# Optimization experiments

Measured on AMD Instinct MI355X. Metric: run time of the kernel, lower is better.

Reference implementation:

```python
import jax, jax.numpy as jnp
import numpy as np


def setup_inputs() -> dict:
    key = jax.random.key(0)
    ks = jax.random.split(key, 9)
    B, C, H, W = 16, 512, 56, 56
    I = C // 2
    return {
        "x": jax.random.normal(ks[0], (B, C, H, W), dtype=jnp.float32),
        "g_w": jax.random.normal(ks[1], (I, C), dtype=jnp.float32) * 0.02,
        "g_b": jax.random.normal(ks[2], (I,), dtype=jnp.float32) * 0.02,
        "theta_w": jax.random.normal(ks[3], (I, C), dtype=jnp.float32) * 0.02,
        "theta_b": jax.random.normal(ks[4], (I,), dtype=jnp.float32) * 0.02,
        "phi_w": jax.random.normal(ks[5], (I, C), dtype=jnp.float32) * 0.02,
        "phi_b": jax.random.normal(ks[6], (I,), dtype=jnp.float32) * 0.02,
        "W_w": jax.random.normal(ks[7], (C, I), dtype=jnp.float32) * 0.02,
        "W_b": jax.random.normal(ks[8], (C,), dtype=jnp.float32) * 0.02,
    }


def reference(x, g_w, g_b, theta_w, theta_b, phi_w, phi_b, W_w, W_b):
    B, C, H, W = x.shape
    N = H * W
    xf = x.reshape(B, C, N)  # flatten spatial -> [B, C, N]
    # 1x1 convs == per-pixel channel matmuls
    g = jnp.einsum('ic,bcn->bin', g_w, xf) + g_b[:, None]        # [B, I, N]
    th = jnp.einsum('ic,bcn->bin', theta_w, xf) + theta_b[:, None]
    ph = jnp.einsum('ic,bcn->bin', phi_w, xf) + phi_b[:, None]
    # Original: y = (theta^T @ phi / N) @ g^T. No softmax -> reassociate:
    # y = theta^T @ ((phi @ g^T) / N), avoiding the [B, N, N] score matrix.
    M = jnp.einsum('bjn,bin->bji', ph, g) / N                    # [B, I, I]
    y = jnp.einsum('bjn,bji->bin', th, M)                        # [B, I, N]
    out = jnp.einsum('ci,bin->bcn', W_w, y) + W_b[:, None]       # [B, C, N]
    return x + out.reshape(B, C, H, W)
```

## Files before the change

### kernel.cpp

```cpp
#include <hip/hip_runtime.h>
#include <stdint.h>


typedef unsigned short ushort_t;
typedef __attribute__((ext_vector_type(8))) short short8;
typedef __attribute__((ext_vector_type(4))) float f32x4;
typedef __attribute__((ext_vector_type(4))) unsigned short us4;
typedef __attribute__((ext_vector_type(8))) unsigned short us8;

#define NSP  3136
#define XNR  3200
#define PLD  3200

#define AS1(p) ((const __attribute__((address_space(1))) void*)(p))
#define AS3(p) ((__attribute__((address_space(3))) void*)(p))

__device__ inline ushort_t f2b(float f) {
  union { float f; uint32_t u; } c; c.f = f;
  uint32_t u = c.u;
  uint32_t r = (u + 0x7fffu + ((u >> 16) & 1u)) >> 16;
  return (ushort_t)r;
}

__global__ __launch_bounds__(512, 2) void g1_8phase(
    const ushort_t* __restrict__ W3,
    const ushort_t* __restrict__ xbase,
    ushort_t* __restrict__ P,
    ushort_t* __restrict__ thT,
    const float* __restrict__ bias)
{
  const int nwg = gridDim.x * gridDim.y * gridDim.z;
  int flat = blockIdx.x + gridDim.x * (blockIdx.y + gridDim.y * blockIdx.z);
  const int q = nwg >> 3;
  int swz = (flat & 7) * q + (flat >> 3);
  const int bx = swz % gridDim.x; int tmp = swz / gridDim.x;
  const int by = tmp % gridDim.y;
  const int b  = tmp / gridDim.y;

  const int m0 = bx * 256;
  const int n0 = by * 256;
  const ushort_t* Ag = W3;
  const ushort_t* Bg = xbase + (size_t)b * XNR * 512;

  const int tid = threadIdx.x;
  const int lane = tid & 63;
  const int wid = tid >> 6;
  const int wm = wid >> 2;
  const int wn = wid & 3;
  const int fr = lane & 15;
  const int fk = lane >> 4;
  const int hB = wn >> 1;
  const int rB0 = (wn & 1) * 64;
  const int s0 = ((fk) ^ (fr & 7)) * 8;
  const int s1 = ((4 | fk) ^ (fr & 7)) * 8;
  const int rth = tid >> 3;
  const int swc = ((tid & 7) ^ ((tid >> 3) & 7)) * 8;

  __shared__ __align__(16) ushort_t SM[65536];
  ushort_t (*As)[2][8192] = (ushort_t(*)[2][8192])(SM);
  ushort_t (*Bs)[2][8192] = (ushort_t(*)[2][8192])(SM + 32768);

  f32x4 acc[8][4];
#pragma unroll
  for (int i = 0; i < 8; ++i)
#pragma unroll
    for (int j = 0; j < 4; ++j) acc[i][j] = f32x4{0.f, 0.f, 0.f, 0.f};

#define STG_A(h, kt, BUF) do { \
    const ushort_t* s_ = Ag + (size_t)(m0 + (h) * 128 + rth) * 512 + (kt) * 64 + swc; \
    __builtin_amdgcn_global_load_lds(AS1(s_), AS3(&As[BUF][h][tid * 8]), 16, 0, 0); \
    __builtin_amdgcn_global_load_lds(AS1(s_ + 64 * 512), AS3(&As[BUF][h][4096 + tid * 8]), 16, 0, 0); \
  } while (0)
#define STG_B(h, kt, BUF) do { \
    const ushort_t* s_ = Bg + (size_t)(n0 + (h) * 128 + rth) * 512 + (kt) * 64 + swc; \
    __builtin_amdgcn_global_load_lds(AS1(s_), AS3(&Bs[BUF][h][tid * 8]), 16, 0, 0); \
    __builtin_amdgcn_global_load_lds(AS1(s_ + 64 * 512), AS3(&Bs[BUF][h][4096 + tid * 8]), 16, 0, 0); \
  } while (0)

#define BARR __builtin_amdgcn_s_barrier()
#define LGKM0 do { asm volatile("s_waitcnt lgkmcnt(0)" ::: "memory"); \
                   __builtin_amdgcn_sched_barrier(0); } while (0)
#define MF16(AF, BF, OFS) do { \
    __builtin_amdgcn_s_setprio(1); \
    _Pragma("unroll") for (int mf_ = 0; mf_ < 4; ++mf_) \
    _Pragma("unroll") for (int nf_ = 0; nf_ < 4; ++nf_) \
      acc[(OFS) + mf_][nf_] = __builtin_amdgcn_mfma_f32_16x16x32_bf16( \
          AF[mf_], BF[nf_], acc[(OFS) + mf_][nf_], 0, 0, 0); \
    __builtin_amdgcn_s_setprio(0); \
  } while (0)

#define TILE(T, CUR, DO_B1, DO_T2, VMN) do { \
    short8 a0[4], a1[4], a2[4], a3[4], b0[4], b1[4]; \
    _Pragma("unroll") for (int i = 0; i < 4; ++i) \
      a0[i] = *(const short8*)&As[CUR][wm][(i * 16 + fr) * 64 + s0]; \
    _Pragma("unroll") for (int i = 0; i < 4; ++i) \
      b0[i] = *(const short8*)&Bs[CUR][hB][(rB0 + i * 16 + fr) * 64 + s0]; \
    if (DO_B1) STG_B(1, (T) + 1, (CUR) ^ 1); \
    BARR; LGKM0; MF16(a0, b0, 0); BARR; \
    _Pragma("unroll") for (int i = 0; i < 4; ++i) \
      a1[i] = *(const short8*)&As[CUR][wm][((i + 4) * 16 + fr) * 64 + s0]; \
    _Pragma("unroll") for (int i = 0; i < 4; ++i) \
      b1[i] = *(const short8*)&Bs[CUR][hB][(rB0 + i * 16 + fr) * 64 + s1]; \
    BARR; LGKM0; MF16(a1, b0, 4); BARR; \
    _Pragma("unroll") for (int i = 0; i < 4; ++i) \
      a2[i] = *(const short8*)&As[CUR][wm][(i * 16 + fr) * 64 + s1]; \
    _Pragma("unroll") for (int i = 0; i < 4; ++i) \
      a3[i] = *(const short8*)&As[CUR][wm][((i + 4) * 16 + fr) * 64 + s1]; \
    if (DO_T2) STG_B(0, (T) + 2, (CUR)); \
    BARR; LGKM0; MF16(a2, b1, 0); BARR; \
    if (DO_T2) { STG_A(0, (T) + 2, (CUR)); STG_A(1, (T) + 2, (CUR)); } \
    if ((VMN) == 6) asm volatile("s_waitcnt vmcnt(6)" ::: "memory"); \
    else if ((VMN) == 0) asm volatile("s_waitcnt vmcnt(0)" ::: "memory"); \
    BARR; MF16(a3, b1, 4); BARR; \
  } while (0)

  asm volatile("s_waitcnt vmcnt(0)" ::: "memory");
  STG_A(0, 0, 0); STG_A(1, 0, 0); STG_B(0, 0, 0); STG_B(1, 0, 0);
  STG_B(0, 1, 1); STG_A(0, 1, 1); STG_A(1, 1, 1);
  asm volatile("s_waitcnt vmcnt(6)" ::: "memory");
  BARR;

  for (int t = 0; t < 6; t += 2) { TILE(t, 0, 1, 1, 6); TILE(t + 1, 1, 1, 1, 6); }
  TILE(6, 0, 1, 0, 0);
  TILE(7, 1, 0, 0, -1);

#undef TILE
#undef STG_A
#undef STG_B

  if (m0 == 512) {
#pragma unroll
    for (int p = 0; p < 2; ++p) {
      if ((wn >> 1) == p) {
        const int lcb = (wn & 1) * 64;
#pragma unroll
        for (int m = 0; m < 8; ++m) {
          int jr = wm * 128 + m * 16 + fk * 4;
#pragma unroll
          for (int n = 0; n < 4; ++n) {
            int lc = lcb + n * 16 + fr;
            us4 o;
#pragma unroll
            for (int r = 0; r < 4; ++r) o[r] = f2b(acc[m][n][r] + bias[512 + jr + r]);
            *reinterpret_cast<us4*>(&SM[lc * 264 + jr]) = o;
          }
        }
      }
      BARR;
#pragma unroll
      for (int it = 0; it < 8; ++it) {
        int idx = it * 512 + tid;
        int lc = idx >> 5, ch = idx & 31;
        int col = n0 + p * 128 + lc;
        if (col < NSP)
          *reinterpret_cast<us8*>(&thT[((size_t)b * NSP + col) * 256 + ch * 8]) =
              *reinterpret_cast<const us8*>(&SM[lc * 264 + ch * 8]);
      }
      BARR;
    }
  } else {
    us8 z = {0, 0, 0, 0, 0, 0, 0, 0};
#pragma unroll
    for (int p = 0; p < 2; ++p) {
      if (wm == p) {
#pragma unroll
        for (int m = 0; m < 8; ++m) {
#pragma unroll
          for (int n = 0; n < 4; ++n) {
            int col = wn * 64 + n * 16 + fr;
#pragma unroll
            for (int r = 0; r < 4; ++r) {
              int lrow = m * 16 + fk * 4 + r;
              SM[lrow * 264 + col] = f2b(acc[m][n][r] + bias[m0 + p * 128 + lrow]);
            }
          }
        }
      }
      BARR;
#pragma unroll
      for (int it = 0; it < 8; ++it) {
        int idx = it * 512 + tid;
        int row = idx >> 5, ch = idx & 31;
        int gcol = n0 + ch * 8;
        if (gcol < PLD) {
          us8 v = (gcol < NSP) ? *reinterpret_cast<const us8*>(&SM[row * 264 + ch * 8]) : z;
          *reinterpret_cast<us8*>(
              &P[(size_t)b * 512 * PLD + (size_t)(m0 + p * 128 + row) * PLD + gcol]) = v;
        }
      }
      BARR;
    }
  }
}

template<int MODE>
__global__ __launch_bounds__(256, 2) void gemm64(
    const ushort_t* __restrict__ Abase,
    const ushort_t* __restrict__ Bbase,
    void* __restrict__ Cbase,
    const float* __restrict__ bias,
    const float* __restrict__ xres)
{
  constexpr int TB = 256;
  constexpr int MR = 4;
  constexpr int WN = 2;
  constexpr int CH = TB / 8;

  const int nwg = gridDim.x * gridDim.y * gridDim.z;
  int flat = blockIdx.x + gridDim.x * (blockIdx.y + gridDim.y * blockIdx.z);
  const int q = nwg >> 3;
  int swz = (flat & 7) * q + (flat >> 3);
  const int bx = swz % gridDim.x; int tmp = swz / gridDim.x;
  const int by = tmp % gridDim.y;
  const int bz = tmp / gridDim.y;

  int b, kc = 0, kbeg, kend, lda, ldb;
  const ushort_t *A, *B;
  if constexpr (MODE == 2) {
    b = bz & 15; kc = bz >> 4;
    A = Abase + (size_t)b * 512 * PLD + (size_t)256 * PLD;
    B = Abase + (size_t)b * 512 * PLD;
    lda = PLD; ldb = PLD; kbeg = kc * 640; kend = kbeg + 640;
  } else if constexpr (MODE == 6) {
    b = bz; A = Abase; lda = 256;
    B = Bbase + (size_t)b * 65536; ldb = 256;
    kbeg = 0; kend = 256;
  } else {
    b = bz; A = Abase + (size_t)b * 131072; lda = 256;
    B = Bbase + (size_t)b * NSP * 256; ldb = 256;
    kbeg = 0; kend = 256;
  }

  const int m0 = bx * 128;
  const int n0 = by * 128;
  const int tid = threadIdx.x;
  const int lane = tid & 63;
  const int wid = tid >> 6;
  const int wm = wid / WN, wn = wid % WN;
  const int fr = lane & 15;
  const int fk = lane >> 4;

  __shared__ __align__(16) ushort_t As[2][128 * 64];
  __shared__ __align__(16) ushort_t Bs[2][128 * 64];

  f32x4 acc[MR][4];
#pragma unroll
  for (int i = 0; i < MR; ++i)
#pragma unroll
    for (int j = 0; j < 4; ++j) acc[i][j] = f32x4{0.f, 0.f, 0.f, 0.f};

  const int srow = tid >> 3;
  const int lsl = (tid & 7) ^ (srow & 7);
  const ushort_t* pa = A + (size_t)(m0 + srow) * lda + kbeg + lsl * 8;
  const ushort_t* pb = B + (size_t)(n0 + srow) * ldb + kbeg + lsl * 8;

#define STAGE(bufi) do {                                                              \
    __builtin_amdgcn_global_load_lds(AS1(pa),                    AS3(&As[bufi][tid * 8]), 16, 0, 0); \
    __builtin_amdgcn_global_load_lds(AS1(pa + (size_t)CH * lda), AS3(&As[bufi][TB * 8 + tid * 8]), 16, 0, 0); \
    __builtin_amdgcn_global_load_lds(AS1(pa + (size_t)2 * CH * lda), AS3(&As[bufi][2 * TB * 8 + tid * 8]), 16, 0, 0); \
    __builtin_amdgcn_global_load_lds(AS1(pa + (size_t)3 * CH * lda), AS3(&As[bufi][3 * TB * 8 + tid * 8]), 16, 0, 0); \
    __builtin_amdgcn_global_load_lds(AS1(pb),                    AS3(&Bs[bufi][tid * 8]), 16, 0, 0); \
    __builtin_amdgcn_global_load_lds(AS1(pb + (size_t)CH * ldb), AS3(&Bs[bufi][TB * 8 + tid * 8]), 16, 0, 0); \
    __builtin_amdgcn_global_load_lds(AS1(pb + (size_t)2 * CH * ldb), AS3(&Bs[bufi][2 * TB * 8 + tid * 8]), 16, 0, 0); \
    __builtin_amdgcn_global_load_lds(AS1(pb + (size_t)3 * CH * ldb), AS3(&Bs[bufi][3 * TB * 8 + tid * 8]), 16, 0, 0); \
    pa += 64; pb += 64;                                                               \
  } while (0)

  const int sw = fr & 7;
  const int s0 = ((0 | fk) ^ sw) * 8;
  const int s1 = ((4 | fk) ^ sw) * 8;
  const int arow = (wm * MR * 16 + fr) * 64;
  const int brow = (wn * 64 + fr) * 64;

  asm volatile("s_waitcnt vmcnt(0)" ::: "memory");
  STAGE(0);

  const int nkt = (kend - kbeg) >> 6;
  for (int t = 0; t < nkt; ++t) {
    const int cur = t & 1;
    if (t + 1 < nkt) {
      STAGE(cur ^ 1);
      asm volatile("s_waitcnt vmcnt(8)" ::: "memory");
    } else {
      asm volatile("s_waitcnt vmcnt(0)" ::: "memory");
    }
    __builtin_amdgcn_s_barrier();
    __builtin_amdgcn_sched_barrier(0);

    short8 bf[4][2];
#pragma unroll
    for (int n = 0; n < 4; ++n) {
      bf[n][0] = *reinterpret_cast<const short8*>(&Bs[cur][brow + n * 1024 + s0]);
      bf[n][1] = *reinterpret_cast<const short8*>(&Bs[cur][brow + n * 1024 + s1]);
    }
    short8 af[4][2];
#pragma unroll
    for (int m = 0; m < 4; ++m) {
      af[m][0] = *reinterpret_cast<const short8*>(&As[cur][arow + m * 1024 + s0]);
      af[m][1] = *reinterpret_cast<const short8*>(&As[cur][arow + m * 1024 + s1]);
    }
    __builtin_amdgcn_s_setprio(1);
#pragma unroll
    for (int m = 0; m < 4; ++m)
#pragma unroll
      for (int n = 0; n < 4; ++n) {
        acc[m][n] = __builtin_amdgcn_mfma_f32_16x16x32_bf16(af[m][0], bf[n][0], acc[m][n], 0, 0, 0);
        acc[m][n] = __builtin_amdgcn_mfma_f32_16x16x32_bf16(af[m][1], bf[n][1], acc[m][n], 0, 0, 0);
      }
    __builtin_amdgcn_s_setprio(0);
    __builtin_amdgcn_s_barrier();
  }
#undef STAGE

  if constexpr (MODE == 2) {
    float* Mf = (float*)Cbase;
#pragma unroll
    for (int m = 0; m < MR; ++m)
#pragma unroll
      for (int n = 0; n < 4; ++n) {
        int gcol = n0 + wn * 64 + n * 16 + fr;
#pragma unroll
        for (int r = 0; r < 4; ++r) {
          int grow = m0 + wm * 64 + m * 16 + fk * 4 + r;
          Mf[((size_t)kc * 16 + b) * 65536 + grow * 256 + gcol] = acc[m][n][r];
        }
      }
  } else if constexpr (MODE == 6) {
    ushort_t* U = (ushort_t*)Cbase;
#pragma unroll
    for (int m = 0; m < MR; ++m)
#pragma unroll
      for (int n = 0; n < 4; ++n) {
        int gcol = n0 + wn * 64 + n * 16 + fr;
#pragma unroll
        for (int r = 0; r < 4; ++r) {
          int grow = m0 + wm * 64 + m * 16 + fk * 4 + r;
          U[(size_t)b * 131072 + grow * 256 + gcol] = f2b(acc[m][n][r]);
        }
      }
  } else {
    float* out = (float*)Cbase;
#pragma unroll
    for (int m = 0; m < MR; ++m)
#pragma unroll
      for (int n = 0; n < 4; ++n) {
        int gcol = n0 + wn * 64 + n * 16 + fr;
        if (gcol < NSP) {
#pragma unroll
          for (int r = 0; r < 4; ++r) {
            int grow = m0 + wm * 64 + m * 16 + fk * 4 + r;
            size_t o = ((size_t)b * 512 + grow) * NSP + gcol;
            out[o] = acc[m][n][r] + bias[grow] + xres[o];
          }
        }
      }
  }
}

__global__ __launch_bounds__(256) void transp_x(const float* __restrict__ x,
                                                ushort_t* __restrict__ xb)
{
  const int nt = blockIdx.x, ct = blockIdx.y, b = blockIdx.z;
  const int t = threadIdx.x;
  const int n0 = nt * 64, c0 = ct * 64;
  __shared__ float Ls[64 * 65];

  const float* xs = x + (size_t)b * 512 * NSP;
#pragma unroll
  for (int p = 0; p < 4; ++p) {
    int cl = p * 16 + (t >> 4);
    int nl = (t & 15) * 4;
    f32x4 v = *reinterpret_cast<const f32x4*>(&xs[(size_t)(c0 + cl) * NSP + n0 + nl]);
    Ls[cl * 65 + nl + 0] = v[0];
    Ls[cl * 65 + nl + 1] = v[1];
    Ls[cl * 65 + nl + 2] = v[2];
    Ls[cl * 65 + nl + 3] = v[3];
  }
  __syncthreads();
#pragma unroll
  for (int it = 0; it < 2; ++it) {
    int idx = it * 256 + t; int nl = idx >> 3, cc = idx & 7;
    us8 o;
#pragma unroll
    for (int j = 0; j < 8; ++j) o[j] = f2b(Ls[(cc * 8 + j) * 65 + nl]);
    *reinterpret_cast<us8*>(&xb[((size_t)b * XNR + n0 + nl) * 512 + c0 + cc * 8]) = o;
  }
}

__global__ __launch_bounds__(256) void prep_weights(
    const float* __restrict__ g_w, const float* __restrict__ ph_w,
    const float* __restrict__ th_w, const float* __restrict__ W_w,
    const float* __restrict__ g_b, const float* __restrict__ ph_b,
    const float* __restrict__ th_b,
    ushort_t* __restrict__ W3, ushort_t* __restrict__ Wwb,
    float* __restrict__ bias3)
{
  int i = blockIdx.x * 256 + threadIdx.x;
  if (i < 393216) {
    int row = i >> 9, col = i & 511;
    float v = (row < 256) ? g_w[row * 512 + col]
            : (row < 512) ? ph_w[(row - 256) * 512 + col]
                          : th_w[(row - 512) * 512 + col];
    W3[i] = f2b(v);
  } else if (i < 524288) {
    Wwb[i - 393216] = f2b(W_w[i - 393216]);
  } else if (i < 525056) {
    int r = i - 524288;
    bias3[r] = (r < 256) ? g_b[r] : (r < 512) ? ph_b[r - 256] : th_b[r - 512];
  }
}

__global__ __launch_bounds__(256) void cvt_M(const float* __restrict__ Mf,
                                             ushort_t* __restrict__ MT)
{
  int i = blockIdx.x * 256 + threadIdx.x;
  const int SL = 1048576;
  float s = 0.f;
#pragma unroll
  for (int k = 0; k < 5; ++k) s += Mf[(size_t)k * SL + i];
  MT[i] = f2b(s * (1.0f / 3136.0f));
}

extern "C" void kernel_launch(void* const* d_in, const int* in_sizes, int n_in,
                              void* d_out, int out_size, void* d_ws, size_t ws_size,
                              hipStream_t stream) {
  const float* x    = (const float*)d_in[0];
  const float* g_w  = (const float*)d_in[1];
  const float* g_b  = (const float*)d_in[2];
  const float* th_w = (const float*)d_in[3];
  const float* th_b = (const float*)d_in[4];
  const float* ph_w = (const float*)d_in[5];
  const float* ph_b = (const float*)d_in[6];
  const float* W_w  = (const float*)d_in[7];
  const float* W_b  = (const float*)d_in[8];

  char* ws = (char*)d_ws;
  ushort_t* xb   = (ushort_t*)(ws + 0);
  float*    Mf2  = (float*)(ws + 0);
  ushort_t* MT2  = (ushort_t*)(ws + 41943040);
  ushort_t* U    = (ushort_t*)(ws + 44040192);
  ushort_t* thT  = (ushort_t*)(ws + 52428800);
  ushort_t* P    = (ushort_t*)(ws + 78118912);
  ushort_t* W3   = (ushort_t*)(ws + 130547712);
  ushort_t* Wwb  = (ushort_t*)(ws + 131334144);
  float*    bias3 = (float*)(ws + 131596288);

  prep_weights<<<2052, 256, 0, stream>>>(g_w, ph_w, th_w, W_w, g_b, ph_b, th_b,
                                         W3, Wwb, bias3);
  transp_x<<<dim3(49, 8, 16), 256, 0, stream>>>(x, xb);

  g1_8phase<<<dim3(3, 13, 16), 512, 0, stream>>>(W3, xb, P, thT, bias3);
  gemm64<2><<<dim3(2, 2, 80), 256, 0, stream>>>(P, nullptr, Mf2, nullptr, nullptr);
  cvt_M<<<4096, 256, 0, stream>>>(Mf2, MT2);
  gemm64<6><<<dim3(4, 2, 16), 256, 0, stream>>>(Wwb, MT2, U, nullptr, nullptr);
  gemm64<4><<<dim3(4, 26, 16), 256, 0, stream>>>(U, thT, d_out, W_b, x);
}
```

Measured before the change: 188.2 us.

## Fold theta projection into output weights so the final GEMM reads x directly

Reassociates the computation so theta is never materialized. The change forms a per-batch effective weight Z = U·theta_w (512x512) and a per-batch bias c0 = U·theta_b + W_b, then runs a big-tile GEMM of Z against the transposed bf16 x with the residual fused in. This removes the theta third of the first projection GEMM and the thT write/read. It adds a small per-batch weight GEMM, a bias kernel, and zero-padding of the x transpose tail, and the final GEMM now has K=512 instead of 256.

```diff
diff --git a/kernel.cpp b/kernel.cpp
--- a/kernel.cpp
+++ b/kernel.cpp
@@ -21,12 +21,14 @@
   uint32_t r = (u + 0x7fffu + ((u >> 16) & 1u)) >> 16;
   return (ushort_t)r;
 }
+__device__ inline float b2f(ushort_t u) {
+  union { uint32_t x; float f; } c; c.x = (uint32_t)u << 16; return c.f;
+}
 
 __global__ __launch_bounds__(512, 2) void g1_8phase(
-    const ushort_t* __restrict__ W3,
+    const ushort_t* __restrict__ W2,
     const ushort_t* __restrict__ xbase,
     ushort_t* __restrict__ P,
-    ushort_t* __restrict__ thT,
     const float* __restrict__ bias)
 {
   const int nwg = gridDim.x * gridDim.y * gridDim.z;
@@ -39,7 +41,7 @@
 
   const int m0 = bx * 256;
   const int n0 = by * 256;
-  const ushort_t* Ag = W3;
+  const ushort_t* Ag = W2;
   const ushort_t* Bg = xbase + (size_t)b * XNR * 512;
 
   const int tid = threadIdx.x;
@@ -128,78 +130,192 @@
 #undef STG_A
 #undef STG_B
 
-  if (m0 == 512) {
-#pragma unroll
-    for (int p = 0; p < 2; ++p) {
-      if ((wn >> 1) == p) {
-        const int lcb = (wn & 1) * 64;
-#pragma unroll
-        for (int m = 0; m < 8; ++m) {
-          int jr = wm * 128 + m * 16 + fk * 4;
-#pragma unroll
-          for (int n = 0; n < 4; ++n) {
-            int lc = lcb + n * 16 + fr;
-            us4 o;
-#pragma unroll
-            for (int r = 0; r < 4; ++r) o[r] = f2b(acc[m][n][r] + bias[512 + jr + r]);
-            *reinterpret_cast<us4*>(&SM[lc * 264 + jr]) = o;
+  us8 z = {0, 0, 0, 0, 0, 0, 0, 0};
+#pragma unroll
+  for (int p = 0; p < 2; ++p) {
+    if (wm == p) {
+#pragma unroll
+      for (int m = 0; m < 8; ++m) {
+#pragma unroll
+        for (int n = 0; n < 4; ++n) {
+          int col = wn * 64 + n * 16 + fr;
+#pragma unroll
+          for (int r = 0; r < 4; ++r) {
+            int lrow = m * 16 + fk * 4 + r;
+            SM[lrow * 264 + col] = f2b(acc[m][n][r] + bias[m0 + p * 128 + lrow]);
           }
         }
       }
-      BARR;
-#pragma unroll
-      for (int it = 0; it < 8; ++it) {
-        int idx = it * 512 + tid;
-        int lc = idx >> 5, ch = idx & 31;
-        int col = n0 + p * 128 + lc;
-        if (col < NSP)
-          *reinterpret_cast<us8*>(&thT[((size_t)b * NSP + col) * 256 + ch * 8]) =
-              *reinterpret_cast<const us8*>(&SM[lc * 264 + ch * 8]);
-      }
-      BARR;
-    }
-  } else {
-    us8 z = {0, 0, 0, 0, 0, 0, 0, 0};
-#pragma unroll
-    for (int p = 0; p < 2; ++p) {
-      if (wm == p) {
-#pragma unroll
-        for (int m = 0; m < 8; ++m) {
-#pragma unroll
-          for (int n = 0; n < 4; ++n) {
-            int col = wn * 64 + n * 16 + fr;
-#pragma unroll
-            for (int r = 0; r < 4; ++r) {
-              int lrow = m * 16 + fk * 4 + r;
-              SM[lrow * 264 + col] = f2b(acc[m][n][r] + bias[m0 + p * 128 + lrow]);
-            }
-          }
+    }
+    BARR;
+#pragma unroll
+    for (int it = 0; it < 8; ++it) {
+      int idx = it * 512 + tid;
+      int row = idx >> 5, ch = idx & 31;
+      int gcol = n0 + ch * 8;
+      if (gcol < PLD) {
+        us8 v = (gcol < NSP) ? *reinterpret_cast<const us8*>(&SM[row * 264 + ch * 8]) : z;
+        *reinterpret_cast<us8*>(
+            &P[(size_t)b * 512 * PLD + (size_t)(m0 + p * 128 + row) * PLD + gcol]) = v;
+      }
+    }
+    BARR;
+  }
+#undef BARR
+#undef LGKM0
+#undef MF16
+}
+
+__global__ __launch_bounds__(512, 2) void gfinal(
+    const ushort_t* __restrict__ Zb,
+    const ushort_t* __restrict__ xbase,
+    float* __restrict__ out,
+    const float* __restrict__ xres,
+    const float* __restrict__ c0)
+{
+  const int nwg = gridDim.x * gridDim.y * gridDim.z;
+  int flat = blockIdx.x + gridDim.x * (blockIdx.y + gridDim.y * blockIdx.z);
+  const int q = nwg >> 3;
+  int swz = (flat & 7) * q + (flat >> 3);
+  const int bx = swz % gridDim.x; int tmp = swz / gridDim.x;
+  const int by = tmp % gridDim.y;
+  const int b  = tmp / gridDim.y;
+
+  const int m0 = bx * 256;
+  const int n0 = by * 256;
+  const ushort_t* Ag = Zb + (size_t)b * 262144;
+  const ushort_t* Bg = xbase + (size_t)b * XNR * 512;
+
+  const int tid = threadIdx.x;
+  const int lane = tid & 63;
+  const int wid = tid >> 6;
+  const int wm = wid >> 2;
+  const int wn = wid & 3;
+  const int fr = lane & 15;
+  const int fk = lane >> 4;
+  const int hB = wn >> 1;
+  const int rB0 = (wn & 1) * 64;
+  const int s0 = ((fk) ^ (fr & 7)) * 8;
+  const int s1 = ((4 | fk) ^ (fr & 7)) * 8;
+  const int rth = tid >> 3;
+  const int swc = ((tid & 7) ^ ((tid >> 3) & 7)) * 8;
+
+  __shared__ __align__(16) ushort_t SM[65536];
+  ushort_t (*As)[2][8192] = (ushort_t(*)[2][8192])(SM);
+  ushort_t (*Bs)[2][8192] = (ushort_t(*)[2][8192])(SM + 32768);
+
+  f32x4 acc[8][4];
+#pragma unroll
+  for (int i = 0; i < 8; ++i)
+#pragma unroll
+    for (int j = 0; j < 4; ++j) acc[i][j] = f32x4{0.f, 0.f, 0.f, 0.f};
+
+#define STG_A(h, kt, BUF) do { \
+    const ushort_t* s_ = Ag + (size_t)(m0 + (h) * 128 + rth) * 512 + (kt) * 64 + swc; \
+    __builtin_amdgcn_global_load_lds(AS1(s_), AS3(&As[BUF][h][tid * 8]), 16, 0, 0); \
+    __builtin_amdgcn_global_load_lds(AS1(s_ + 64 * 512), AS3(&As[BUF][h][4096 + tid * 8]), 16, 0, 0); \
+  } while (0)
+#define STG_B(h, kt, BUF) do { \
+    const ushort_t* s_ = Bg + (size_t)(n0 + (h) * 128 + rth) * 512 + (kt) * 64 + swc; \
+    __builtin_amdgcn_global_load_lds(AS1(s_), AS3(&Bs[BUF][h][tid * 8]), 16, 0, 0); \
+    __builtin_amdgcn_global_load_lds(AS1(s_ + 64 * 512), AS3(&Bs[BUF][h][4096 + tid * 8]), 16, 0, 0); \
+  } while (0)
+
+#define BARR __builtin_amdgcn_s_barrier()
+#define LGKM0 do { asm volatile("s_waitcnt lgkmcnt(0)" ::: "memory"); \
+                   __builtin_amdgcn_sched_barrier(0); } while (0)
+#define MF16(AF, BF, OFS) do { \
+    __builtin_amdgcn_s_setprio(1); \
+    _Pragma("unroll") for (int mf_ = 0; mf_ < 4; ++mf_) \
+    _Pragma("unroll") for (int nf_ = 0; nf_ < 4; ++nf_) \
+      acc[(OFS) + mf_][nf_] = __builtin_amdgcn_mfma_f32_16x16x32_bf16( \
+          AF[mf_], BF[nf_], acc[(OFS) + mf_][nf_], 0, 0, 0); \
+    __builtin_amdgcn_s_setprio(0); \
+  } while (0)
+
+#define TILE(T, CUR, DO_B1, DO_T2, VMN) do { \
+    short8 a0[4], a1[4], a2[4], a3[4], b0[4], b1[4]; \
+    _Pragma("unroll") for (int i = 0; i < 4; ++i) \
+      a0[i] = *(const short8*)&As[CUR][wm][(i * 16 + fr) * 64 + s0]; \
+    _Pragma("unroll") for (int i = 0; i < 4; ++i) \
+      b0[i] = *(const short8*)&Bs[CUR][hB][(rB0 + i * 16 + fr) * 64 + s0]; \
+    if (DO_B1) STG_B(1, (T) + 1, (CUR) ^ 1); \
+    BARR; LGKM0; MF16(a0, b0, 0); BARR; \
+    _Pragma("unroll") for (int i = 0; i < 4; ++i) \
+      a1[i] = *(const short8*)&As[CUR][wm][((i + 4) * 16 + fr) * 64 + s0]; \
+    _Pragma("unroll") for (int i = 0; i < 4; ++i) \
+      b1[i] = *(const short8*)&Bs[CUR][hB][(rB0 + i * 16 + fr) * 64 + s1]; \
+    BARR; LGKM0; MF16(a1, b0, 4); BARR; \
+    _Pragma("unroll") for (int i = 0; i < 4; ++i) \
+      a2[i] = *(const short8*)&As[CUR][wm][(i * 16 + fr) * 64 + s1]; \
+    _Pragma("unroll") for (int i = 0; i < 4; ++i) \
+      a3[i] = *(const short8*)&As[CUR][wm][((i + 4) * 16 + fr) * 64 + s1]; \
+    if (DO_T2) STG_B(0, (T) + 2, (CUR)); \
+    BARR; LGKM0; MF16(a2, b1, 0); BARR; \
+    if (DO_T2) { STG_A(0, (T) + 2, (CUR)); STG_A(1, (T) + 2, (CUR)); } \
+    if ((VMN) == 6) asm volatile("s_waitcnt vmcnt(6)" ::: "memory"); \
+    else if ((VMN) == 0) asm volatile("s_waitcnt vmcnt(0)" ::: "memory"); \
+    BARR; MF16(a3, b1, 4); BARR; \
+  } while (0)
+
+  asm volatile("s_waitcnt vmcnt(0)" ::: "memory");
+  STG_A(0, 0, 0); STG_A(1, 0, 0); STG_B(0, 0, 0); STG_B(1, 0, 0);
+  STG_B(0, 1, 1); STG_A(0, 1, 1); STG_A(1, 1, 1);
+  asm volatile("s_waitcnt vmcnt(6)" ::: "memory");
+  BARR;
+
+  for (int t = 0; t < 6; t += 2) { TILE(t, 0, 1, 1, 6); TILE(t + 1, 1, 1, 1, 6); }
+  TILE(6, 0, 1, 0, 0);
+  TILE(7, 1, 0, 0, -1);
+
+#undef TILE
+#undef STG_A
+#undef STG_B
+
+  float* SMf = (float*)SM;
+  const float* c0v = c0 + (size_t)b * 512;
+#pragma unroll
+  for (int p = 0; p < 2; ++p) {
+    if (wm == p) {
+#pragma unroll
+      for (int m = 0; m < 8; ++m)
+#pragma unroll
+        for (int n = 0; n < 4; ++n) {
+          int col = wn * 64 + n * 16 + fr;
+#pragma unroll
+          for (int r = 0; r < 4; ++r)
+            SMf[(m * 16 + fk * 4 + r) * 256 + col] = acc[m][n][r];
         }
-      }
-      BARR;
-#pragma unroll
-      for (int it = 0; it < 8; ++it) {
-        int idx = it * 512 + tid;
-        int row = idx >> 5, ch = idx & 31;
-        int gcol = n0 + ch * 8;
-        if (gcol < PLD) {
-          us8 v = (gcol < NSP) ? *reinterpret_cast<const us8*>(&SM[row * 264 + ch * 8]) : z;
-          *reinterpret_cast<us8*>(
-              &P[(size_t)b * 512 * PLD + (size_t)(m0 + p * 128 + row) * PLD + gcol]) = v;
-        }
-      }
-      BARR;
-    }
-  }
+    }
+    BARR;
+#pragma unroll
+    for (int it = 0; it < 16; ++it) {
+      int idx = it * 512 + tid;
+      int row = idx >> 6, ch = idx & 63;
+      int gcol = n0 + ch * 4;
+      if (gcol < NSP) {
+        int grow = m0 + p * 128 + row;
+        size_t o = ((size_t)b * 512 + grow) * (size_t)NSP + gcol;
+        f32x4 v = *reinterpret_cast<const f32x4*>(&SMf[row * 256 + ch * 4]);
+        f32x4 xr = *reinterpret_cast<const f32x4*>(&xres[o]);
+        float bi = c0v[grow];
+        f32x4 ov = {v[0] + bi + xr[0], v[1] + bi + xr[1],
+                    v[2] + bi + xr[2], v[3] + bi + xr[3]};
+        *reinterpret_cast<f32x4*>(&out[o]) = ov;
+      }
+    }
+    BARR;
+  }
+#undef BARR
+#undef LGKM0
+#undef MF16
 }
 
 template<int MODE>
 __global__ __launch_bounds__(256, 2) void gemm64(
     const ushort_t* __restrict__ Abase,
     const ushort_t* __restrict__ Bbase,
-    void* __restrict__ Cbase,
-    const float* __restrict__ bias,
-    const float* __restrict__ xres)
+    void* __restrict__ Cbase)
 {
   constexpr int TB = 256;
   constexpr int MR = 4;
@@ -214,7 +330,7 @@
   const int by = tmp % gridDim.y;
   const int bz = tmp / gridDim.y;
 
-  int b, kc = 0, kbeg, kend, lda, ldb;
+  int b = bz, kc = 0, kbeg = 0, kend, lda, ldb;
   const ushort_t *A, *B;
   if constexpr (MODE == 2) {
     b = bz & 15; kc = bz >> 4;
@@ -222,13 +338,13 @@
     B = Abase + (size_t)b * 512 * PLD;
     lda = PLD; ldb = PLD; kbeg = kc * 640; kend = kbeg + 640;
   } else if constexpr (MODE == 6) {
-    b = bz; A = Abase; lda = 256;
+    A = Abase; lda = 256;
     B = Bbase + (size_t)b * 65536; ldb = 256;
-    kbeg = 0; kend = 256;
+    kend = 256;
   } else {
-    b = bz; A = Abase + (size_t)b * 131072; lda = 256;
-    B = Bbase + (size_t)b * NSP * 256; ldb = 256;
-    kbeg = 0; kend = 256;
+    A = Abase + (size_t)b * 131072; lda = 256;
+    B = Bbase; ldb = 256;
+    kend = 256;
   }
 
   const int m0 = bx * 128;
@@ -339,19 +455,16 @@
         }
       }
   } else {
-    float* out = (float*)Cbase;
+    ushort_t* Z = (ushort_t*)Cbase;
 #pragma unroll
     for (int m = 0; m < MR; ++m)
 #pragma unroll
       for (int n = 0; n < 4; ++n) {
         int gcol = n0 + wn * 64 + n * 16 + fr;
-        if (gcol < NSP) {
-#pragma unroll
-          for (int r = 0; r < 4; ++r) {
-            int grow = m0 + wm * 64 + m * 16 + fk * 4 + r;
-            size_t o = ((size_t)b * 512 + grow) * NSP + gcol;
-            out[o] = acc[m][n][r] + bias[grow] + xres[o];
-          }
+#pragma unroll
+        for (int r = 0; r < 4; ++r) {
+          int grow = m0 + wm * 64 + m * 16 + fk * 4 + r;
+          Z[(size_t)b * 262144 + (size_t)grow * 512 + gcol] = f2b(acc[m][n][r]);
         }
       }
   }
@@ -365,6 +478,15 @@
   const int n0 = nt * 64, c0 = ct * 64;
   __shared__ float Ls[64 * 65];
 
+  if (nt == 49) {
+    us8 z = {0, 0, 0, 0, 0, 0, 0, 0};
+#pragma unroll
+    for (int it = 0; it < 2; ++it) {
+      int idx = it * 256 + t; int nl = idx >> 3, cc = idx & 7;
+      *reinterpret_cast<us8*>(&xb[((size_t)b * XNR + n0 + nl) * 512 + c0 + cc * 8]) = z;
+    }
+    return;
+  }
   const float* xs = x + (size_t)b * 512 * NSP;
 #pragma unroll
   for (int p = 0; p < 4; ++p) {
@@ -391,22 +513,22 @@
     const float* __restrict__ g_w, const float* __restrict__ ph_w,
     const float* __restrict__ th_w, const float* __restrict__ W_w,
     const float* __restrict__ g_b, const float* __restrict__ ph_b,
-    const float* __restrict__ th_b,
-    ushort_t* __restrict__ W3, ushort_t* __restrict__ Wwb,
-    float* __restrict__ bias3)
+    ushort_t* __restrict__ W2, ushort_t* __restrict__ TwT,
+    ushort_t* __restrict__ Wwb, float* __restrict__ bias2)
 {
   int i = blockIdx.x * 256 + threadIdx.x;
-  if (i < 393216) {
+  if (i < 262144) {
     int row = i >> 9, col = i & 511;
-    float v = (row < 256) ? g_w[row * 512 + col]
-            : (row < 512) ? ph_w[(row - 256) * 512 + col]
-                          : th_w[(row - 512) * 512 + col];
-    W3[i] = f2b(v);
+    float v = (row < 256) ? g_w[row * 512 + col] : ph_w[(row - 256) * 512 + col];
+    W2[i] = f2b(v);
+  } else if (i < 393216) {
+    int j = i - 262144; int ct = j >> 8; int k = j & 255;
+    TwT[j] = f2b(th_w[(size_t)k * 512 + ct]);
   } else if (i < 524288) {
     Wwb[i - 393216] = f2b(W_w[i - 393216]);
-  } else if (i < 525056) {
+  } else if (i < 524800) {
     int r = i - 524288;
-    bias3[r] = (r < 256) ? g_b[r] : (r < 512) ? ph_b[r - 256] : th_b[r - 512];
+    bias2[r] = (r < 256) ? g_b[r] : ph_b[r - 256];
   }
 }
 
@@ -419,6 +541,20 @@
 #pragma unroll
   for (int k = 0; k < 5; ++k) s += Mf[(size_t)k * SL + i];
   MT[i] = f2b(s * (1.0f / 3136.0f));
+}
+
+__global__ __launch_bounds__(256) void u3k(const ushort_t* __restrict__ U,
+                                           const float* __restrict__ th_b,
+                                           const float* __restrict__ W_b,
+                                           float* __restrict__ c0)
+{
+  int i = blockIdx.x * 256 + threadIdx.x;
+  int c = i & 511;
+  const ushort_t* Ur = U + (size_t)i * 256;
+  float a = 0.f;
+#pragma unroll 4
+  for (int j = 0; j < 256; ++j) a += b2f(Ur[j]) * th_b[j];
+  c0[i] = a + W_b[c];
 }
 
 extern "C" void kernel_launch(void* const* d_in, const int* in_sizes, int n_in,
@@ -436,22 +572,26 @@
 
   char* ws = (char*)d_ws;
   ushort_t* xb   = (ushort_t*)(ws + 0);
-  float*    Mf2  = (float*)(ws + 0);
-  ushort_t* MT2  = (ushort_t*)(ws + 41943040);
-  ushort_t* U    = (ushort_t*)(ws + 44040192);
-  ushort_t* thT  = (ushort_t*)(ws + 52428800);
-  ushort_t* P    = (ushort_t*)(ws + 78118912);
-  ushort_t* W3   = (ushort_t*)(ws + 130547712);
-  ushort_t* Wwb  = (ushort_t*)(ws + 131334144);
-  float*    bias3 = (float*)(ws + 131596288);
-
-  prep_weights<<<2052, 256, 0, stream>>>(g_w, ph_w, th_w, W_w, g_b, ph_b, th_b,
-                                         W3, Wwb, bias3);
-  transp_x<<<dim3(49, 8, 16), 256, 0, stream>>>(x, xb);
-
-  g1_8phase<<<dim3(3, 13, 16), 512, 0, stream>>>(W3, xb, P, thT, bias3);
-  gemm64<2><<<dim3(2, 2, 80), 256, 0, stream>>>(P, nullptr, Mf2, nullptr, nullptr);
+  ushort_t* P    = (ushort_t*)(ws + 52428800);
+  ushort_t* U    = (ushort_t*)(ws + 52428800);
+  ushort_t* Z    = (ushort_t*)(ws + 56623104);
+  float*    Mf2  = (float*)(ws + 104857600);
+  ushort_t* MT2  = (ushort_t*)(ws + 125829120);
+  ushort_t* W2   = (ushort_t*)(ws + 127926272);
+  ushort_t* TwT  = (ushort_t*)(ws + 128450560);
+  ushort_t* Wwb  = (ushort_t*)(ws + 128712704);
+  float*    bias2 = (float*)(ws + 128974848);
+  float*    c0   = (float*)(ws + 128976896);
+
+  prep_weights<<<2051, 256, 0, stream>>>(g_w, ph_w, th_w, W_w, g_b, ph_b,
+                                         W2, TwT, Wwb, bias2);
+  transp_x<<<dim3(50, 8, 16), 256, 0, stream>>>(x, xb);
+
+  g1_8phase<<<dim3(2, 13, 16), 512, 0, stream>>>(W2, xb, P, bias2);
+  gemm64<2><<<dim3(2, 2, 80), 256, 0, stream>>>(P, nullptr, Mf2);
   cvt_M<<<4096, 256, 0, stream>>>(Mf2, MT2);
-  gemm64<6><<<dim3(4, 2, 16), 256, 0, stream>>>(Wwb, MT2, U, nullptr, nullptr);
-  gemm64<4><<<dim3(4, 26, 16), 256, 0, stream>>>(U, thT, d_out, W_b, x);
-}
+  gemm64<6><<<dim3(4, 2, 16), 256, 0, stream>>>(Wwb, MT2, U);
+  gemm64<7><<<dim3(4, 4, 16), 256, 0, stream>>>(U, TwT, Z);
+  u3k<<<32, 256, 0, stream>>>(U, th_b, W_b, c0);
+  gfinal<<<dim3(2, 13, 16), 512, 0, stream>>>(Z, xb, (float*)d_out, x, c0);
+}
```

After: 186.8 us. Within noise of the previous version (-0.8%).
